# Kernel tuning notes

Measured on AMD Instinct MI355X. Metric: run time of the kernel, lower is better.

## Reference

```python
import jax, jax.numpy as jnp
import numpy as np

N_NODES = 50000
N_EDGES = 800000
IN_DIM = 128
OUT_DIM = 64


def setup_inputs() -> dict:
    key = jax.random.key(0)
    k1, k2, k3, k4, k5, k6 = jax.random.split(key, 6)
    x = jax.random.normal(k1, (N_NODES, IN_DIM), dtype=jnp.float32)
    edge_row = jax.random.randint(k2, (N_EDGES,), 0, N_NODES, dtype=jnp.int32)
    edge_col = jax.random.randint(k3, (N_EDGES,), 0, N_NODES, dtype=jnp.int32)
    edge_val = jax.random.uniform(k4, (N_EDGES,), dtype=jnp.float32)
    stdv = 1.0 / np.sqrt(OUT_DIM)
    w = jax.random.uniform(k5, (IN_DIM, OUT_DIM), minval=-stdv, maxval=stdv, dtype=jnp.float32)
    b = jax.random.uniform(k6, (OUT_DIM,), minval=-stdv, maxval=stdv, dtype=jnp.float32)
    return {"x": x, "edge_row": edge_row, "edge_col": edge_col, "edge_val": edge_val, "w": w, "b": b}


def reference(x, edge_row, edge_col, edge_val, w, b):
    # dense projection: [N, in_dim] @ [in_dim, out_dim] -> [N, out_dim]
    hidden = x @ w
    # SpMM: out[r] = sum_e val[e] * hidden[col[e]] for edges with row[e] == r
    msg = hidden[edge_col] * edge_val[:, None]          # [E, out_dim]
    out = jax.ops.segment_sum(msg, edge_row, num_segments=N_NODES)
    return jax.nn.relu(out + b)
```

## Files before the change

kernel.cpp:

```cpp
#include <hip/hip_runtime.h>

#define N_NODES 50000
#define N_EDGES 800000
#define IN_DIM 128
#define OUT_DIM 64
#define CAP 64
#define PARTS 8
#define ROWS_PER_PART 6250
#define EDGES_PER_CHUNK 3125

#define OFF_HID 0u
#define OFF_DEG 6400000u
#define OFF_BKT 6600192u

typedef short short8 __attribute__((ext_vector_type(8)));
typedef float f32x4 __attribute__((ext_vector_type(4)));

__device__ __forceinline__ unsigned short bf_rne(float f) {
    unsigned u = __float_as_uint(f);
    u += 0x7fffu + ((u >> 16) & 1u);
    return (unsigned short)(u >> 16);
}
__device__ __forceinline__ float bf_lo(unsigned u) { return __uint_as_float(u << 16); }
__device__ __forceinline__ float bf_hi(unsigned u) { return __uint_as_float(u & 0xffff0000u); }

__global__ __launch_bounds__(256) void gemm_kernel(const float* __restrict__ x,
                                                   const float* __restrict__ w,
                                                   unsigned short* __restrict__ hidb) {
    __shared__ unsigned short wperm[16 * 64 * 8];
    __shared__ unsigned short obuf[4][16 * 64];

    const int tid = threadIdx.x;
    const int lane = tid & 63;
    const int wid = tid >> 6;

    for (int s = tid; s < 16 * 64 * 8; s += 256) {
        const int f = s >> 9;
        const int ln = (s >> 3) & 63;
        const int j = s & 7;
        const int c = f >> 2, t = f & 3;
        const int k = c * 32 + (ln >> 4) * 8 + j;
        const int n = t * 16 + (ln & 15);
        wperm[s] = bf_rne(w[k * OUT_DIM + n]);
    }
    __syncthreads();

    const int group = blockIdx.x * 4 + wid;
    if (group < N_NODES / 16) {
        short8 bf[16];
        #pragma unroll
        for (int f = 0; f < 16; ++f)
            bf[f] = *(const short8*)&wperm[(f * 64 + lane) * 8];

        const int node0 = group * 16;
        f32x4 acc[4] = {{0, 0, 0, 0}, {0, 0, 0, 0}, {0, 0, 0, 0}, {0, 0, 0, 0}};

        #pragma unroll
        for (int c = 0; c < 4; ++c) {
            const float* xr = x + (size_t)(node0 + (lane & 15)) * IN_DIM + c * 32 + (lane >> 4) * 8;
            const float4 a0 = *(const float4*)xr;
            const float4 a1 = *(const float4*)(xr + 4);
            short8 af;
            af[0] = (short)bf_rne(a0.x); af[1] = (short)bf_rne(a0.y);
            af[2] = (short)bf_rne(a0.z); af[3] = (short)bf_rne(a0.w);
            af[4] = (short)bf_rne(a1.x); af[5] = (short)bf_rne(a1.y);
            af[6] = (short)bf_rne(a1.z); af[7] = (short)bf_rne(a1.w);
            #pragma unroll
            for (int t = 0; t < 4; ++t)
                acc[t] = __builtin_amdgcn_mfma_f32_16x16x32_bf16(af, bf[c * 4 + t], acc[t], 0, 0, 0);
        }

        #pragma unroll
        for (int t = 0; t < 4; ++t)
            #pragma unroll
            for (int r = 0; r < 4; ++r)
                obuf[wid][((lane >> 4) * 4 + r) * 64 + t * 16 + (lane & 15)] = bf_rne(acc[t][r]);
        const uint4 o0 = *(const uint4*)&obuf[wid][lane * 16];
        const uint4 o1 = *(const uint4*)&obuf[wid][lane * 16 + 8];
        char* dst = (char*)hidb + (size_t)node0 * (OUT_DIM * 2) + lane * 32;
        *(uint4*)dst = o0;
        *(uint4*)(dst + 16) = o1;
    }
}

__global__ __launch_bounds__(256) void bucket_kernel(const int* __restrict__ erow,
                                                     const int* __restrict__ ecol,
                                                     const float* __restrict__ eval,
                                                     int* __restrict__ deg,
                                                     int2* __restrict__ bucket) {
    const int part = blockIdx.x & (PARTS - 1);
    const int chunk = blockIdx.x >> 3;
    const int rlo = part * ROWS_PER_PART;
    const int e0 = chunk * EDGES_PER_CHUNK;
    for (int i = threadIdx.x; i < EDGES_PER_CHUNK; i += 256) {
        const int e = e0 + i;
        const int r = erow[e];
        const int c = ecol[e];
        const float v = eval[e];
        if ((unsigned)(r - rlo) < (unsigned)ROWS_PER_PART) {
            const int pos = atomicAdd(&deg[r], 1);
            if (pos < CAP) bucket[(size_t)r * CAP + pos] = make_int2(c, __float_as_int(v));
        }
    }
}

__global__ __launch_bounds__(256) void agg_kernel(const unsigned short* __restrict__ hidb,
                                                  const int* __restrict__ deg,
                                                  const int2* __restrict__ bucket,
                                                  const float* __restrict__ b,
                                                  float* __restrict__ out) {
    const int g = blockIdx.x * 4 + (threadIdx.x >> 6);
    const int lane = threadIdx.x & 63;
    const int half = lane >> 5;
    const int l = lane & 31;
    const int row = g * 2 + half;
    if (row >= N_NODES) return;

    const int d = min(deg[row], CAP);
    const int2* __restrict__ ep = bucket + (size_t)row * CAP;

    float acc0 = 0.f, acc1 = 0.f;
    int i = 0;
    for (; i + 4 <= d; i += 4) {
        const int2 p0 = ep[i], p1 = ep[i + 1], p2 = ep[i + 2], p3 = ep[i + 3];
        const unsigned u0 = *(const unsigned*)&hidb[(size_t)p0.x * OUT_DIM + 2 * l];
        const unsigned u1 = *(const unsigned*)&hidb[(size_t)p1.x * OUT_DIM + 2 * l];
        const unsigned u2 = *(const unsigned*)&hidb[(size_t)p2.x * OUT_DIM + 2 * l];
        const unsigned u3 = *(const unsigned*)&hidb[(size_t)p3.x * OUT_DIM + 2 * l];
        const float v0 = __int_as_float(p0.y), v1 = __int_as_float(p1.y);
        const float v2 = __int_as_float(p2.y), v3 = __int_as_float(p3.y);
        acc0 = fmaf(v0, bf_lo(u0), acc0); acc1 = fmaf(v0, bf_hi(u0), acc1);
        acc0 = fmaf(v1, bf_lo(u1), acc0); acc1 = fmaf(v1, bf_hi(u1), acc1);
        acc0 = fmaf(v2, bf_lo(u2), acc0); acc1 = fmaf(v2, bf_hi(u2), acc1);
        acc0 = fmaf(v3, bf_lo(u3), acc0); acc1 = fmaf(v3, bf_hi(u3), acc1);
    }
    for (; i < d; ++i) {
        const int2 p = ep[i];
        const unsigned u = *(const unsigned*)&hidb[(size_t)p.x * OUT_DIM + 2 * l];
        const float v = __int_as_float(p.y);
        acc0 = fmaf(v, bf_lo(u), acc0); acc1 = fmaf(v, bf_hi(u), acc1);
    }
    const float2 bb = *(const float2*)&b[2 * l];
    float2 o;
    o.x = fmaxf(acc0 + bb.x, 0.f);
    o.y = fmaxf(acc1 + bb.y, 0.f);
    *(float2*)&out[(size_t)row * OUT_DIM + 2 * l] = o;
}

extern "C" void kernel_launch(void* const* d_in, const int* in_sizes, int n_in,
                              void* d_out, int out_size, void* d_ws, size_t ws_size,
                              hipStream_t stream) {
    const float* x    = (const float*)d_in[0];
    const int*   erow = (const int*)d_in[1];
    const int*   ecol = (const int*)d_in[2];
    const float* eval = (const float*)d_in[3];
    const float* w    = (const float*)d_in[4];
    const float* b    = (const float*)d_in[5];
    float* out = (float*)d_out;

    char* ws = (char*)d_ws;
    unsigned short* hidb = (unsigned short*)(ws + OFF_HID);
    int*  deg    = (int*)(ws + OFF_DEG);
    int2* bucket = (int2*)(ws + OFF_BKT);

    hipMemsetAsync(deg, 0, N_NODES * sizeof(int), stream);

    gemm_kernel<<<(N_NODES / 16 + 3) / 4, 256, 0, stream>>>(x, w, hidb);

    bucket_kernel<<<256 * PARTS, 256, 0, stream>>>(erow, ecol, eval, deg, bucket);

    agg_kernel<<<(N_NODES / 2 + 3) / 4, 256, 0, stream>>>(hidb, deg, bucket, b, out);
}
```

Before: 156.5 us.

## Fuse GEMM and bucketing into one launch; rework aggregation with shuffled edge lists

The bucket-fill and GEMM kernels are merged into one launch, with block index choosing the role, so the two independent stages run concurrently and one launch is saved. The GEMM part reuses a single shared buffer for the weight permutation and the output staging, which needs an extra barrier. The aggregation kernel now gives 16 lanes to each row, 4 features per lane. It loads the edge list cooperatively and broadcasts it with shuffles, and issues 8 independent gathers per step to expose more memory parallelism. The cost is wasted lanes when degrees differ within a wave, since the loop runs to the wave-wide maximum degree.

```diff
diff --git a/kernel.cpp b/kernel.cpp
--- a/kernel.cpp
+++ b/kernel.cpp
@@ -8,6 +8,8 @@
 #define PARTS 8
 #define ROWS_PER_PART 6250
 #define EDGES_PER_CHUNK 3125
+#define BUCKET_BLOCKS (256 * PARTS)
+#define GEMM_BLOCKS 782
 
 #define OFF_HID 0u
 #define OFF_DEG 6400000u
@@ -24,11 +26,31 @@
 __device__ __forceinline__ float bf_lo(unsigned u) { return __uint_as_float(u << 16); }
 __device__ __forceinline__ float bf_hi(unsigned u) { return __uint_as_float(u & 0xffff0000u); }
 
-__global__ __launch_bounds__(256) void gemm_kernel(const float* __restrict__ x,
-                                                   const float* __restrict__ w,
-                                                   unsigned short* __restrict__ hidb) {
-    __shared__ unsigned short wperm[16 * 64 * 8];
-    __shared__ unsigned short obuf[4][16 * 64];
+__global__ __launch_bounds__(256) void fused_kernel(
+        const float* __restrict__ x, const float* __restrict__ w,
+        unsigned short* __restrict__ hidb,
+        const int* __restrict__ erow, const int* __restrict__ ecol,
+        const float* __restrict__ eval,
+        int* __restrict__ deg, int2* __restrict__ bucket) {
+    if (blockIdx.x < BUCKET_BLOCKS) {
+        const int part = blockIdx.x & (PARTS - 1);
+        const int chunk = blockIdx.x >> 3;
+        const int rlo = part * ROWS_PER_PART;
+        const int e0 = chunk * EDGES_PER_CHUNK;
+        for (int i = threadIdx.x; i < EDGES_PER_CHUNK; i += 256) {
+            const int e = e0 + i;
+            const int r = erow[e];
+            const int c = ecol[e];
+            const float v = eval[e];
+            if ((unsigned)(r - rlo) < (unsigned)ROWS_PER_PART) {
+                const int pos = atomicAdd(&deg[r], 1);
+                if (pos < CAP) bucket[(size_t)r * CAP + pos] = make_int2(c, __float_as_int(v));
+            }
+        }
+        return;
+    }
+
+    __shared__ __attribute__((aligned(16))) unsigned short smem[16 * 64 * 8];
 
     const int tid = threadIdx.x;
     const int lane = tid & 63;
@@ -41,17 +63,22 @@
         const int c = f >> 2, t = f & 3;
         const int k = c * 32 + (ln >> 4) * 8 + j;
         const int n = t * 16 + (ln & 15);
-        wperm[s] = bf_rne(w[k * OUT_DIM + n]);
+        smem[s] = bf_rne(w[k * OUT_DIM + n]);
     }
     __syncthreads();
 
-    const int group = blockIdx.x * 4 + wid;
-    if (group < N_NODES / 16) {
-        short8 bf[16];
+    const int group = (blockIdx.x - BUCKET_BLOCKS) * 4 + wid;
+    const bool act = group < N_NODES / 16;
+
+    short8 bf[16];
+    if (act) {
         #pragma unroll
         for (int f = 0; f < 16; ++f)
-            bf[f] = *(const short8*)&wperm[(f * 64 + lane) * 8];
-
+            bf[f] = *(const short8*)&smem[(f * 64 + lane) * 8];
+    }
+    __syncthreads();
+
+    if (act) {
         const int node0 = group * 16;
         f32x4 acc[4] = {{0, 0, 0, 0}, {0, 0, 0, 0}, {0, 0, 0, 0}, {0, 0, 0, 0}};
 
@@ -70,37 +97,44 @@
                 acc[t] = __builtin_amdgcn_mfma_f32_16x16x32_bf16(af, bf[c * 4 + t], acc[t], 0, 0, 0);
         }
 
+        unsigned short* obuf = smem + wid * 1024;
         #pragma unroll
         for (int t = 0; t < 4; ++t)
             #pragma unroll
             for (int r = 0; r < 4; ++r)
-                obuf[wid][((lane >> 4) * 4 + r) * 64 + t * 16 + (lane & 15)] = bf_rne(acc[t][r]);
-        const uint4 o0 = *(const uint4*)&obuf[wid][lane * 16];
-        const uint4 o1 = *(const uint4*)&obuf[wid][lane * 16 + 8];
+                obuf[((lane >> 4) * 4 + r) * 64 + t * 16 + (lane & 15)] = bf_rne(acc[t][r]);
+        const uint4 o0 = *(const uint4*)&obuf[lane * 16];
+        const uint4 o1 = *(const uint4*)&obuf[lane * 16 + 8];
         char* dst = (char*)hidb + (size_t)node0 * (OUT_DIM * 2) + lane * 32;
         *(uint4*)dst = o0;
         *(uint4*)(dst + 16) = o1;
     }
 }
 
-__global__ __launch_bounds__(256) void bucket_kernel(const int* __restrict__ erow,
-                                                     const int* __restrict__ ecol,
-                                                     const float* __restrict__ eval,
-                                                     int* __restrict__ deg,
-                                                     int2* __restrict__ bucket) {
-    const int part = blockIdx.x & (PARTS - 1);
-    const int chunk = blockIdx.x >> 3;
-    const int rlo = part * ROWS_PER_PART;
-    const int e0 = chunk * EDGES_PER_CHUNK;
-    for (int i = threadIdx.x; i < EDGES_PER_CHUNK; i += 256) {
-        const int e = e0 + i;
-        const int r = erow[e];
-        const int c = ecol[e];
-        const float v = eval[e];
-        if ((unsigned)(r - rlo) < (unsigned)ROWS_PER_PART) {
-            const int pos = atomicAdd(&deg[r], 1);
-            if (pos < CAP) bucket[(size_t)r * CAP + pos] = make_int2(c, __float_as_int(v));
-        }
+__device__ __forceinline__ void proc8(const unsigned short* __restrict__ hidb,
+                                      int2 P, int base, int eoff,
+                                      int q, int l, int d, float4& acc) {
+    unsigned long long u[8];
+    float vv[8];
+    #pragma unroll
+    for (int e = 0; e < 8; ++e) {
+        const int src = q * 16 + eoff + e;
+        int c = __shfl(P.x, src);
+        const int vi = __shfl(P.y, src);
+        const bool act = (base + eoff + e) < d;
+        c = act ? c : 0;
+        vv[e] = act ? __int_as_float(vi) : 0.f;
+        u[e] = *(const unsigned long long*)&hidb[(size_t)c * OUT_DIM + 4 * l];
+    }
+    #pragma unroll
+    for (int e = 0; e < 8; ++e) {
+        const float v = vv[e];
+        const unsigned ulo = (unsigned)u[e];
+        const unsigned uhi = (unsigned)(u[e] >> 32);
+        acc.x = fmaf(v, bf_lo(ulo), acc.x);
+        acc.y = fmaf(v, bf_hi(ulo), acc.y);
+        acc.z = fmaf(v, bf_lo(uhi), acc.z);
+        acc.w = fmaf(v, bf_hi(uhi), acc.w);
     }
 }
 
@@ -109,42 +143,42 @@
                                                   const int2* __restrict__ bucket,
                                                   const float* __restrict__ b,
                                                   float* __restrict__ out) {
-    const int g = blockIdx.x * 4 + (threadIdx.x >> 6);
-    const int lane = threadIdx.x & 63;
-    const int half = lane >> 5;
-    const int l = lane & 31;
-    const int row = g * 2 + half;
-    if (row >= N_NODES) return;
+    const int tid = threadIdx.x;
+    const int lane = tid & 63;
+    const int wid = tid >> 6;
+    const int q = lane >> 4;
+    const int l = lane & 15;
+    const int row = blockIdx.x * 16 + wid * 4 + q;
 
     const int d = min(deg[row], CAP);
     const int2* __restrict__ ep = bucket + (size_t)row * CAP;
 
-    float acc0 = 0.f, acc1 = 0.f;
-    int i = 0;
-    for (; i + 4 <= d; i += 4) {
-        const int2 p0 = ep[i], p1 = ep[i + 1], p2 = ep[i + 2], p3 = ep[i + 3];
-        const unsigned u0 = *(const unsigned*)&hidb[(size_t)p0.x * OUT_DIM + 2 * l];
-        const unsigned u1 = *(const unsigned*)&hidb[(size_t)p1.x * OUT_DIM + 2 * l];
-        const unsigned u2 = *(const unsigned*)&hidb[(size_t)p2.x * OUT_DIM + 2 * l];
-        const unsigned u3 = *(const unsigned*)&hidb[(size_t)p3.x * OUT_DIM + 2 * l];
-        const float v0 = __int_as_float(p0.y), v1 = __int_as_float(p1.y);
-        const float v2 = __int_as_float(p2.y), v3 = __int_as_float(p3.y);
-        acc0 = fmaf(v0, bf_lo(u0), acc0); acc1 = fmaf(v0, bf_hi(u0), acc1);
-        acc0 = fmaf(v1, bf_lo(u1), acc0); acc1 = fmaf(v1, bf_hi(u1), acc1);
-        acc0 = fmaf(v2, bf_lo(u2), acc0); acc1 = fmaf(v2, bf_hi(u2), acc1);
-        acc0 = fmaf(v3, bf_lo(u3), acc0); acc1 = fmaf(v3, bf_hi(u3), acc1);
-    }
-    for (; i < d; ++i) {
-        const int2 p = ep[i];
-        const unsigned u = *(const unsigned*)&hidb[(size_t)p.x * OUT_DIM + 2 * l];
-        const float v = __int_as_float(p.y);
-        acc0 = fmaf(v, bf_lo(u), acc0); acc1 = fmaf(v, bf_hi(u), acc1);
-    }
-    const float2 bb = *(const float2*)&b[2 * l];
-    float2 o;
-    o.x = fmaxf(acc0 + bb.x, 0.f);
-    o.y = fmaxf(acc1 + bb.y, 0.f);
-    *(float2*)&out[(size_t)row * OUT_DIM + 2 * l] = o;
+    int dmax = d;
+    dmax = max(dmax, __shfl_xor(dmax, 16));
+    dmax = max(dmax, __shfl_xor(dmax, 32));
+
+    const int2 pa = ep[l];
+    const int2 pb = ep[16 + l];
+
+    float4 acc = make_float4(0.f, 0.f, 0.f, 0.f);
+
+    proc8(hidb, pa, 0, 0, q, l, d, acc);
+    if (dmax > 8)  proc8(hidb, pa, 0, 8, q, l, d, acc);
+    if (dmax > 16) proc8(hidb, pb, 16, 0, q, l, d, acc);
+    if (dmax > 24) proc8(hidb, pb, 16, 8, q, l, d, acc);
+    for (int base = 32; base < dmax; base += 16) {
+        const int2 pc = ep[base + l];
+        proc8(hidb, pc, base, 0, q, l, d, acc);
+        if (dmax > base + 8) proc8(hidb, pc, base, 8, q, l, d, acc);
+    }
+
+    const float4 bb = *(const float4*)&b[4 * l];
+    float4 o;
+    o.x = fmaxf(acc.x + bb.x, 0.f);
+    o.y = fmaxf(acc.y + bb.y, 0.f);
+    o.z = fmaxf(acc.z + bb.z, 0.f);
+    o.w = fmaxf(acc.w + bb.w, 0.f);
+    *(float4*)&out[(size_t)row * OUT_DIM + 4 * l] = o;
 }
 
 extern "C" void kernel_launch(void* const* d_in, const int* in_sizes, int n_in,
@@ -165,9 +199,8 @@
 
     hipMemsetAsync(deg, 0, N_NODES * sizeof(int), stream);
 
-    gemm_kernel<<<(N_NODES / 16 + 3) / 4, 256, 0, stream>>>(x, w, hidb);
-
-    bucket_kernel<<<256 * PARTS, 256, 0, stream>>>(erow, ecol, eval, deg, bucket);
-
-    agg_kernel<<<(N_NODES / 2 + 3) / 4, 256, 0, stream>>>(hidb, deg, bucket, b, out);
-}
+    fused_kernel<<<BUCKET_BLOCKS + GEMM_BLOCKS, 256, 0, stream>>>(
+        x, w, hidb, erow, ecol, eval, deg, bucket);
+
+    agg_kernel<<<N_NODES / 16, 256, 0, stream>>>(hidb, deg, bucket, b, out);
+}
```

New measurement: 145.9 us. -6.8%, faster.
